# Kernel tuning notes

Hardware: AMD Instinct MI355X
Metric: run time of the kernel (lower is better)

The kernel has to match this reference:

```python
import jax, jax.numpy as jnp
import numpy as np

T, D_IN, H, KV, HD = 1024, 2048, 32, 8, 64
GROUP = H // KV  # 4
EPS = 1e-6


def _rmsnorm(x, w):
    inv_rms = jax.lax.rsqrt(jnp.mean(x * x, axis=-1, keepdims=True) + EPS)
    return x * inv_rms * w


def _rope(x, cos, sin):
    # x: [heads, T, HD]; cos/sin: [T, HD]
    hd = x.shape[-1]
    x1, x2 = x[..., : hd // 2], x[..., hd // 2 :]
    rotated = jnp.concatenate([-x2, x1], axis=-1)
    return x * cos[None, :, :] + rotated * sin[None, :, :]


def setup_inputs() -> dict:
    key = jax.random.key(0)
    ks = jax.random.split(key, 6)
    x = jax.random.normal(ks[0], (T, D_IN), dtype=jnp.float32)
    # RoPE tables (cos/sin over [T, HD])
    inv_freq = 1.0 / (10000.0 ** (np.arange(0, HD, 2, dtype=np.float64) / HD))
    ang = np.arange(T, dtype=np.float64)[:, None] * inv_freq[None, :]
    emb = np.concatenate([ang, ang], axis=-1)
    cos = jnp.asarray(np.cos(emb), dtype=jnp.float32)
    sin = jnp.asarray(np.sin(emb), dtype=jnp.float32)
    # causal mask: True above diagonal -> masked to -inf
    mask = jnp.triu(jnp.ones((T, T), dtype=jnp.bool_), k=1)
    # kaiming_normal fan_in (relu): std = sqrt(2/fan_in)
    Wq = jax.random.normal(ks[1], (H * HD, D_IN), jnp.float32) * (2.0 / D_IN) ** 0.5
    Wk = jax.random.normal(ks[2], (KV * HD, D_IN), jnp.float32) * (2.0 / D_IN) ** 0.5
    Wv = jax.random.normal(ks[3], (KV * HD, D_IN), jnp.float32) * (2.0 / D_IN) ** 0.5
    Wo = jax.random.normal(ks[4], (D_IN, H * HD), jnp.float32) * (2.0 / (H * HD)) ** 0.5
    q_norm_w = jnp.ones((HD,), jnp.float32)
    k_norm_w = jnp.ones((HD,), jnp.float32)
    one = jnp.ones((1,), jnp.float32)
    return {
        "x": x, "scale_x": one, "mask": mask,
        "cos": cos, "scale_cos": one, "sin": sin, "scale_sin": one,
        "Wq": Wq, "Wk": Wk, "Wv": Wv, "Wo": Wo,
        "q_norm_w": q_norm_w, "k_norm_w": k_norm_w,
    }


def reference(x, scale_x, mask, cos, scale_cos, sin, scale_sin,
              Wq, Wk, Wv, Wo, q_norm_w, k_norm_w):
    num_tokens = x.shape[0]
    # QKV projections
    q = (x @ Wq.T).reshape(num_tokens, H, HD).transpose(1, 0, 2)   # [H, T, HD]
    k = (x @ Wk.T).reshape(num_tokens, KV, HD).transpose(1, 0, 2)  # [KV, T, HD]
    v = (x @ Wv.T).reshape(num_tokens, KV, HD).transpose(1, 0, 2)  # [KV, T, HD]
    # qk_norm
    q = _rmsnorm(q, q_norm_w)
    k = _rmsnorm(k, k_norm_w)
    # RoPE
    q = _rope(q, cos, sin)
    k = _rope(k, cos, sin)
    # expand KV groups to all heads (repeat_interleave along head axis)
    k = jnp.repeat(k, GROUP, axis=0)  # [H, T, HD]
    v = jnp.repeat(v, GROUP, axis=0)  # [H, T, HD]
    # attention scores
    qk = jnp.einsum("htd,hsd->hts", q, k) / (HD ** 0.5)
    qk = jnp.where(mask[None, :, :], -jnp.inf, qk)
    attn = jax.nn.softmax(qk, axis=-1)
    out = jnp.einsum("hts,hsd->htd", attn, v)          # [H, T, HD]
    out = out.transpose(1, 0, 2).reshape(num_tokens, H * HD)
    return out @ Wo.T  # [T, D_IN]
```

## Files before the change

kernel.cpp:

```cpp
#include <hip/hip_runtime.h>

typedef __bf16 bf16x8 __attribute__((ext_vector_type(8)));
typedef float f32x4 __attribute__((ext_vector_type(4)));

#define T_TOK 1024
#define DIN   2048
#define NH    32
#define NKV   8
#define HD    64

__device__ __forceinline__ unsigned short f2bf(float f) {
  unsigned int u = __float_as_uint(f);
  unsigned int r = (u + 0x7fffu + ((u >> 16) & 1u)) >> 16;
  return (unsigned short)r;
}

__device__ __forceinline__ void glds16(const void* g, void* lds) {
  __builtin_amdgcn_global_load_lds(
      (const __attribute__((address_space(1))) void*)g,
      (__attribute__((address_space(3))) void*)lds, 16, 0, 0);
}

__global__ __launch_bounds__(256) void k_cvt_all(
    const float* __restrict__ x,  const float* __restrict__ wq,
    const float* __restrict__ wk, const float* __restrict__ wv,
    const float* __restrict__ wo, unsigned short* __restrict__ xb,
    unsigned short* __restrict__ wqkv, unsigned short* __restrict__ wob) {
  const long NX = 1l << 21, NWQ = 1l << 22, NWK = 1l << 20, NWV = 1l << 20;
  long i4 = ((long)blockIdx.x * blockDim.x + threadIdx.x) * 4;
  const float* src;
  unsigned short* dst;
  long off;
  if (i4 < NX)                       { src = x;  dst = xb;   off = i4; }
  else if (i4 < NX + NWQ)            { src = wq; dst = wqkv; off = i4 - NX; }
  else if (i4 < NX + NWQ + NWK)      { src = wk; dst = wqkv + NWQ; off = i4 - NX - NWQ; }
  else if (i4 < NX + NWQ + NWK + NWV){ src = wv; dst = wqkv + NWQ + NWK; off = i4 - NX - NWQ - NWK; }
  else                               { src = wo; dst = wob;  off = i4 - NX - NWQ - NWK - NWV; }
  float4 v = *reinterpret_cast<const float4*>(src + off);
  ushort4 o;
  o.x = f2bf(v.x); o.y = f2bf(v.y); o.z = f2bf(v.z); o.w = f2bf(v.w);
  *reinterpret_cast<ushort4*>(dst + off) = o;
}

template<int BM, int BN>
__global__ __launch_bounds__(256) void k_gemm3(
    const unsigned short* __restrict__ A, const unsigned short* __restrict__ B,
    float* __restrict__ C, int N, int K) {
  constexpr int NI = BM / 32;
  constexpr int NJ = BN / 32;
  __shared__ unsigned short As[4][BM * 64];
  __shared__ unsigned short Bs[4][BN * 64];
  const int lane = threadIdx.x & 63;
  const int wave = threadIdx.x >> 6;
  const int wm = wave >> 1, wn = wave & 1;
  const int lr = lane & 15, lk = lane >> 4;
  const int brow = blockIdx.y * BM;
  const int bcol = blockIdx.x * BN;

  const int srow = lane >> 3;
  const int scol = ((lane & 7) ^ srow) * 8;
  const unsigned short* Ag = A + (long)(brow + srow) * K + scol;
  const unsigned short* Bg = B + (long)(bcol + srow) * K + scol;

  f32x4 acc[NI][NJ];
#pragma unroll
  for (int i = 0; i < NI; i++)
#pragma unroll
    for (int j = 0; j < NJ; j++) acc[i][j] = (f32x4){0.f, 0.f, 0.f, 0.f};

  const int swz = (lr & 7) << 4;
  const int nt = K / 64;

#define GSTAGE(buf, tt) do {                                                   \
    const int kk_ = (tt) * 64;                                                 \
    _Pragma("unroll") for (int i_ = 0; i_ < NI; i_++) {                        \
      int strip = i_ * 4 + wave;                                               \
      glds16(Ag + (long)strip * 8 * K + kk_, (char*)As[buf] + strip * 1024);   \
    }                                                                          \
    _Pragma("unroll") for (int i_ = 0; i_ < NJ; i_++) {                        \
      int strip = i_ * 4 + wave;                                               \
      glds16(Bg + (long)strip * 8 * K + kk_, (char*)Bs[buf] + strip * 1024);   \
    }                                                                          \
  } while (0)

  GSTAGE(0, 0);
  GSTAGE(1, 1);
  GSTAGE(2, 2);

  for (int t = 0; t < nt; t++) {
    if (t + 2 < nt)      { asm volatile("s_waitcnt vmcnt(16)" ::: "memory"); }
    else if (t + 1 < nt) { asm volatile("s_waitcnt vmcnt(8)"  ::: "memory"); }
    else                 { asm volatile("s_waitcnt vmcnt(0)"  ::: "memory"); }
    __builtin_amdgcn_sched_barrier(0);
    __builtin_amdgcn_s_barrier();
    if (t + 3 < nt) GSTAGE((t + 3) & 3, t + 3);
    const int cur = t & 3;
#pragma unroll
    for (int s = 0; s < 2; s++) {
      bf16x8 a[NI], b[NJ];
#pragma unroll
      for (int i = 0; i < NI; i++) {
        int row = wm * (BM / 2) + i * 16 + lr;
        a[i] = *reinterpret_cast<const bf16x8*>(
            (const char*)As[cur] + row * 128 + ((s * 64 + lk * 16) ^ swz));
      }
#pragma unroll
      for (int j = 0; j < NJ; j++) {
        int row = wn * (BN / 2) + j * 16 + lr;
        b[j] = *reinterpret_cast<const bf16x8*>(
            (const char*)Bs[cur] + row * 128 + ((s * 64 + lk * 16) ^ swz));
      }
      __builtin_amdgcn_s_setprio(1);
#pragma unroll
      for (int i = 0; i < NI; i++)
#pragma unroll
        for (int j = 0; j < NJ; j++)
          acc[i][j] = __builtin_amdgcn_mfma_f32_16x16x32_bf16(a[i], b[j], acc[i][j], 0, 0, 0);
      __builtin_amdgcn_s_setprio(0);
    }
  }
#undef GSTAGE

#pragma unroll
  for (int i = 0; i < NI; i++)
#pragma unroll
    for (int j = 0; j < NJ; j++)
#pragma unroll
      for (int p = 0; p < 4; p++)
        C[(long)(brow + wm * (BM / 2) + i * 16 + lk * 4 + p) * N +
          (bcol + wn * (BN / 2) + j * 16 + lr)] = acc[i][j][p];
}

__global__ void k_norm_rope(const float* __restrict__ qkv_lin,
                            unsigned short* __restrict__ qb, unsigned short* __restrict__ kb,
                            const float* __restrict__ cosT, const float* __restrict__ sinT,
                            const float* __restrict__ qw, const float* __restrict__ kw) {
  int gw = (blockIdx.x * blockDim.x + threadIdx.x) >> 6;
  int lane = threadIdx.x & 63;
  int t = gw / (NH + NKV);
  int hh = gw % (NH + NKV);
  if (t >= T_TOK) return;
  const float* base;
  unsigned short* ob;
  const float* w;
  if (hh < NH) {
    base = qkv_lin + (long)t * 3072 + hh * HD;
    ob   = qb + (long)t * (NH * HD) + hh * HD;
    w = qw;
  } else {
    int kh = hh - NH;
    base = qkv_lin + (long)t * 3072 + 2048 + kh * HD;
    ob   = kb + (long)t * (NKV * HD) + kh * HD;
    w = kw;
  }
  float v = base[lane];
  float ss = v * v;
#pragma unroll
  for (int off = 1; off < 64; off <<= 1) ss += __shfl_xor(ss, off);
  float xn = v * rsqrtf(ss * (1.0f / HD) + 1e-6f) * w[lane];
  float other = __shfl_xor(xn, 32);
  float c = cosT[t * HD + lane], s = sinT[t * HD + lane];
  ob[lane] = f2bf(xn * c + (lane < 32 ? -other : other) * s);
}

__global__ __launch_bounds__(256) void k_vt(const float* __restrict__ qkv_lin,
                                            unsigned short* __restrict__ out) {
  __shared__ float t[32][33];
  int tx = threadIdx.x & 31, ty = threadIdx.x >> 5;
  int r0 = blockIdx.y * 32;
  int c0 = blockIdx.x * 32;
#pragma unroll
  for (int r = 0; r < 4; r++)
    t[ty + r * 8][tx] = qkv_lin[(long)(r0 + ty + r * 8) * 3072 + 2560 + c0 + tx];
  __syncthreads();
#pragma unroll
  for (int r = 0; r < 4; r++)
    out[(long)(c0 + ty + r * 8) * 1024 + r0 + tx] = f2bf(t[tx][ty + r * 8]);
}

__global__ __launch_bounds__(256) void k_flash(
    const unsigned short* __restrict__ qb, const unsigned short* __restrict__ kb,
    const unsigned short* __restrict__ vtb, unsigned short* __restrict__ ao) {
  __shared__ unsigned short Ks[4][64 * 64];
  __shared__ unsigned short Vs[4][64 * 64];
  __shared__ unsigned short plds[4][16 * 64];
  const int rb = 63 - blockIdx.x;
  const int kvh = blockIdx.y;
  const int lane = threadIdx.x & 63;
  const int wave = threadIdx.x >> 6;
  const int h = kvh * 4 + wave;
  const int lr = lane & 15, lk = lane >> 4;
  const int qrow = rb * 16;
  const int qt = rb >> 2;
  const int qrel = (rb & 3) * 16 + lr;
  const int pswz = (lr & 7) << 4;
  char* pbase = (char*)plds[wave];
  const float SC = 0.125f * 1.44269504f;
  const f32x4 z4 = {0.f, 0.f, 0.f, 0.f};

  const int srow = lane >> 3;
  const int scol = ((lane & 7) ^ srow) * 8;

#define STAGE(buf, tt) do {                                                    \
    _Pragma("unroll") for (int s_ = 0; s_ < 2; s_++) {                         \
      int strip = s_ * 4 + wave;                                               \
      glds16(kb + (long)((tt) * 64 + strip * 8 + srow) * 512 + kvh * 64 + scol,\
             (char*)Ks[buf] + strip * 1024);                                   \
      glds16(vtb + (long)(kvh * 64 + strip * 8 + srow) * 1024 + (tt) * 64 + scol,\
             (char*)Vs[buf] + strip * 1024);                                   \
    }                                                                          \
  } while (0)

  const unsigned short* qp = qb + (long)(qrow + lr) * (NH * HD) + h * HD + lk * 8;
  bf16x8 qa0 = *reinterpret_cast<const bf16x8*>(qp);
  bf16x8 qa1 = *reinterpret_cast<const bf16x8*>(qp + 32);

  f32x4 o[4];
#pragma unroll
  for (int f = 0; f < 4; f++) o[f] = z4;
  float m2 = -3.0e38f;
  float lp = 0.f;

  const int ntiles = qt + 1;
  STAGE(0, 0);
  if (ntiles > 1) STAGE(1, 1);
  if (ntiles > 2) STAGE(2, 2);

  for (int t = 0; t < ntiles; t++) {
    if (t + 2 < ntiles)      { asm volatile("s_waitcnt vmcnt(8)" ::: "memory"); }
    else if (t + 1 < ntiles) { asm volatile("s_waitcnt vmcnt(4)" ::: "memory"); }
    else                     { asm volatile("s_waitcnt vmcnt(0)" ::: "memory"); }
    __builtin_amdgcn_sched_barrier(0);
    __builtin_amdgcn_s_barrier();
    if (t + 3 < ntiles) STAGE((t + 3) & 3, t + 3);
    const int cur = t & 3;
    bf16x8 kf0[4], kf1[4];
#pragma unroll
    for (int f = 0; f < 4; f++) {
      const char* kbase = (const char*)Ks[cur] + (f * 16 + lr) * 128;
      kf0[f] = *reinterpret_cast<const bf16x8*>(kbase + ((lk * 16) ^ pswz));
      kf1[f] = *reinterpret_cast<const bf16x8*>(kbase + ((64 + lk * 16) ^ pswz));
    }
    f32x4 sacc[4];
    __builtin_amdgcn_s_setprio(1);
#pragma unroll
    for (int f = 0; f < 4; f++) {
      sacc[f] = __builtin_amdgcn_mfma_f32_16x16x32_bf16(kf0[f], qa0, z4, 0, 0, 0);
      sacc[f] = __builtin_amdgcn_mfma_f32_16x16x32_bf16(kf1[f], qa1, sacc[f], 0, 0, 0);
    }
    __builtin_amdgcn_s_setprio(0);
    const bool diag = (t == qt);
    float tmax = -3.0e38f;
#pragma unroll
    for (int f = 0; f < 4; f++)
#pragma unroll
      for (int p = 0; p < 4; p++) {
        float s_ = sacc[f][p] * SC;
        if (diag && (f * 16 + lk * 4 + p) > qrel) s_ = -3.0e38f;
        sacc[f][p] = s_;
        tmax = fmaxf(tmax, s_);
      }
    tmax = fmaxf(tmax, __shfl_xor(tmax, 16));
    tmax = fmaxf(tmax, __shfl_xor(tmax, 32));
    float mn = fmaxf(m2, tmax);
    float r = exp2f(m2 - mn);
    m2 = mn;
    float rp[4];
#pragma unroll
    for (int p = 0; p < 4; p++)
      rp[p] = __shfl(r, (lane & 48) | (lk * 4 + p));
    float ps = 0.f;
#pragma unroll
    for (int f = 0; f < 4; f++) {
      float e0 = exp2f(sacc[f][0] - mn), e1 = exp2f(sacc[f][1] - mn);
      float e2 = exp2f(sacc[f][2] - mn), e3 = exp2f(sacc[f][3] - mn);
      ps += (e0 + e1) + (e2 + e3);
      uint2 pk;
      pk.x = (unsigned)f2bf(e0) | ((unsigned)f2bf(e1) << 16);
      pk.y = (unsigned)f2bf(e2) | ((unsigned)f2bf(e3) << 16);
      *reinterpret_cast<uint2*>(pbase + lr * 128 + ((f * 32 + lk * 8) ^ pswz)) = pk;
    }
    lp = lp * r + ps;
#pragma unroll
    for (int fd = 0; fd < 4; fd++)
#pragma unroll
      for (int p = 0; p < 4; p++) o[fd][p] *= rp[p];
    bf16x8 vfr[8];
#pragma unroll
    for (int fd = 0; fd < 4; fd++) {
      const char* vbase = (const char*)Vs[cur] + (fd * 16 + lr) * 128;
      vfr[fd]     = *reinterpret_cast<const bf16x8*>(vbase + ((lk * 16) ^ pswz));
      vfr[4 + fd] = *reinterpret_cast<const bf16x8*>(vbase + ((64 + lk * 16) ^ pswz));
    }
    __builtin_amdgcn_s_setprio(1);
#pragma unroll
    for (int ks = 0; ks < 2; ks++) {
      bf16x8 pa = *reinterpret_cast<const bf16x8*>(
          pbase + lr * 128 + ((ks * 64 + lk * 16) ^ pswz));
#pragma unroll
      for (int fd = 0; fd < 4; fd++)
        o[fd] = __builtin_amdgcn_mfma_f32_16x16x32_bf16(pa, vfr[ks * 4 + fd], o[fd], 0, 0, 0);
    }
    __builtin_amdgcn_s_setprio(0);
  }
#undef STAGE

  lp += __shfl_xor(lp, 16);
  lp += __shfl_xor(lp, 32);
  float lo[4];
#pragma unroll
  for (int p = 0; p < 4; p++) lo[p] = __shfl(lp, (lane & 48) | (lk * 4 + p));
#pragma unroll
  for (int fd = 0; fd < 4; fd++)
#pragma unroll
    for (int p = 0; p < 4; p++) {
      int qg = qrow + lk * 4 + p;
      int d = fd * 16 + lr;
      ao[(long)qg * (NH * HD) + h * HD + d] = f2bf(o[fd][p] / lo[p]);
    }
}

extern "C" void kernel_launch(void* const* d_in, const int* in_sizes, int n_in,
                              void* d_out, int out_size, void* d_ws, size_t ws_size,
                              hipStream_t stream) {
  const float* x    = (const float*)d_in[0];
  const float* cosT = (const float*)d_in[3];
  const float* sinT = (const float*)d_in[5];
  const float* Wq   = (const float*)d_in[7];
  const float* Wk   = (const float*)d_in[8];
  const float* Wv   = (const float*)d_in[9];
  const float* Wo   = (const float*)d_in[10];
  const float* qw   = (const float*)d_in[11];
  const float* kw   = (const float*)d_in[12];
  float* out = (float*)d_out;

  char* ws = (char*)d_ws;
  unsigned short* xb    = (unsigned short*)(ws);
  unsigned short* Wqkv  = (unsigned short*)(ws + (4u << 20));
  unsigned short* Wob   = (unsigned short*)(ws + (16u << 20));
  float* qkv_lin = (float*)(ws + (24u << 20));
  unsigned short* qbb = (unsigned short*)(ws + (36u << 20));
  unsigned short* kbb = (unsigned short*)(ws + (40u << 20));
  unsigned short* vtb = (unsigned short*)(ws + (41u << 20));
  unsigned short* ao  = (unsigned short*)(ws + (42u << 20));

  k_cvt_all<<<12288, 256, 0, stream>>>(x, Wq, Wk, Wv, Wo, xb, Wqkv, Wob);

  k_gemm3<128, 128><<<dim3(24, 8), 256, 0, stream>>>(xb, Wqkv, qkv_lin, 3072, 2048);

  k_norm_rope<<<(T_TOK * (NH + NKV) * 64) / 256, 256, 0, stream>>>(
      qkv_lin, qbb, kbb, cosT, sinT, qw, kw);

  k_vt<<<dim3(16, 32), 256, 0, stream>>>(qkv_lin, vtb);

  k_flash<<<dim3(64, 8), 256, 0, stream>>>(qbb, kbb, vtb, ao);

  k_gemm3<128, 128><<<dim3(16, 8), 256, 0, stream>>>(ao, Wob, out, 2048, 2048);
}
```

Measured before the change: 218.9 us.

## Fuse QK RMSNorm, RoPE and V transpose into QKV GEMM epilogue

Moves the Q/K RMSNorm and RoPE plus the V transpose into the QKV GEMM epilogue, dropping the fp32 qkv_lin intermediate and two kernel launches. GEMM tiles shrink to 64x128 with a 3-stage instead of 4-stage LDS pipeline, doubling grid size for better CU occupancy on both GEMMs. The epilogue now does cross-lane shuffles and scattered bf16 stores. Lower LDS use allows more resident blocks, but the shallower prefetch exposes more memory latency.

```diff
diff --git a/kernel.cpp b/kernel.cpp
--- a/kernel.cpp
+++ b/kernel.cpp
@@ -42,14 +42,19 @@
   *reinterpret_cast<ushort4*>(dst + off) = o;
 }
 
-template<int BM, int BN>
+template<int BM, int BN, int MODE>
 __global__ __launch_bounds__(256) void k_gemm3(
     const unsigned short* __restrict__ A, const unsigned short* __restrict__ B,
-    float* __restrict__ C, int N, int K) {
+    float* __restrict__ C, int N, int K,
+    unsigned short* __restrict__ qb, unsigned short* __restrict__ kbo,
+    unsigned short* __restrict__ vtb, const float* __restrict__ cosT,
+    const float* __restrict__ sinT, const float* __restrict__ qw,
+    const float* __restrict__ kw) {
   constexpr int NI = BM / 32;
   constexpr int NJ = BN / 32;
-  __shared__ unsigned short As[4][BM * 64];
-  __shared__ unsigned short Bs[4][BN * 64];
+  static_assert(NI + NJ == 6, "vmcnt literals assume 6 loads/batch/wave");
+  __shared__ unsigned short As[3][BM * 64];
+  __shared__ unsigned short Bs[3][BN * 64];
   const int lane = threadIdx.x & 63;
   const int wave = threadIdx.x >> 6;
   const int wm = wave >> 1, wn = wave & 1;
@@ -85,16 +90,14 @@
 
   GSTAGE(0, 0);
   GSTAGE(1, 1);
-  GSTAGE(2, 2);
 
   for (int t = 0; t < nt; t++) {
-    if (t + 2 < nt)      { asm volatile("s_waitcnt vmcnt(16)" ::: "memory"); }
-    else if (t + 1 < nt) { asm volatile("s_waitcnt vmcnt(8)"  ::: "memory"); }
-    else                 { asm volatile("s_waitcnt vmcnt(0)"  ::: "memory"); }
+    if (t + 1 < nt) { asm volatile("s_waitcnt vmcnt(6)" ::: "memory"); }
+    else            { asm volatile("s_waitcnt vmcnt(0)" ::: "memory"); }
     __builtin_amdgcn_sched_barrier(0);
     __builtin_amdgcn_s_barrier();
-    if (t + 3 < nt) GSTAGE((t + 3) & 3, t + 3);
-    const int cur = t & 3;
+    if (t + 2 < nt) GSTAGE((t + 2) % 3, t + 2);
+    const int cur = t % 3;
 #pragma unroll
     for (int s = 0; s < 2; s++) {
       bf16x8 a[NI], b[NJ];
@@ -121,61 +124,68 @@
   }
 #undef GSTAGE
 
-#pragma unroll
-  for (int i = 0; i < NI; i++)
-#pragma unroll
-    for (int j = 0; j < NJ; j++)
-#pragma unroll
-      for (int p = 0; p < 4; p++)
-        C[(long)(brow + wm * (BM / 2) + i * 16 + lk * 4 + p) * N +
-          (bcol + wn * (BN / 2) + j * 16 + lr)] = acc[i][j][p];
-}
-
-__global__ void k_norm_rope(const float* __restrict__ qkv_lin,
-                            unsigned short* __restrict__ qb, unsigned short* __restrict__ kb,
-                            const float* __restrict__ cosT, const float* __restrict__ sinT,
-                            const float* __restrict__ qw, const float* __restrict__ kw) {
-  int gw = (blockIdx.x * blockDim.x + threadIdx.x) >> 6;
-  int lane = threadIdx.x & 63;
-  int t = gw / (NH + NKV);
-  int hh = gw % (NH + NKV);
-  if (t >= T_TOK) return;
-  const float* base;
-  unsigned short* ob;
-  const float* w;
-  if (hh < NH) {
-    base = qkv_lin + (long)t * 3072 + hh * HD;
-    ob   = qb + (long)t * (NH * HD) + hh * HD;
-    w = qw;
+  if constexpr (MODE == 1) {
+    const int colbase = bcol + wn * 64;
+    if (colbase < 2560) {
+      const bool isQ = (colbase < 2048);
+      const float* w = isQ ? qw : kw;
+      unsigned short* dst = isQ ? qb : kbo;
+      const int dN = isQ ? (NH * HD) : (NKV * HD);
+      const int dcol = isQ ? colbase : colbase - 2048;
+      float wv[NJ];
+#pragma unroll
+      for (int j = 0; j < NJ; j++) wv[j] = w[j * 16 + lr];
+#pragma unroll
+      for (int i = 0; i < NI; i++) {
+#pragma unroll
+        for (int p = 0; p < 4; p++) {
+          float s2 = 0.f;
+#pragma unroll
+          for (int j = 0; j < NJ; j++) s2 += acc[i][j][p] * acc[i][j][p];
+          s2 += __shfl_xor(s2, 1);
+          s2 += __shfl_xor(s2, 2);
+          s2 += __shfl_xor(s2, 4);
+          s2 += __shfl_xor(s2, 8);
+          const float inv = rsqrtf(s2 * (1.0f / HD) + 1e-6f);
+          const int t = brow + wm * (BM / 2) + i * 16 + lk * 4 + p;
+#pragma unroll
+          for (int j = 0; j < NJ; j++) {
+            const int hd = j * 16 + lr;
+            const float xn = acc[i][j][p] * inv * wv[j];
+            const int jp = (j < 2) ? j + 2 : j - 2;
+            float rot = acc[i][jp][p] * inv * wv[jp];
+            if (j < 2) rot = -rot;
+            const float c = cosT[t * HD + hd], s = sinT[t * HD + hd];
+            dst[(long)t * dN + dcol + hd] = f2bf(xn * c + rot * s);
+          }
+        }
+      }
+    } else {
+#pragma unroll
+      for (int i = 0; i < NI; i++) {
+        const int t0 = brow + wm * (BM / 2) + i * 16 + lk * 4;
+#pragma unroll
+        for (int j = 0; j < NJ; j++) {
+          const int c = colbase - 2560 + j * 16 + lr;
+          ushort4 pk;
+          pk.x = f2bf(acc[i][j][0]);
+          pk.y = f2bf(acc[i][j][1]);
+          pk.z = f2bf(acc[i][j][2]);
+          pk.w = f2bf(acc[i][j][3]);
+          *reinterpret_cast<ushort4*>(vtb + (long)c * T_TOK + t0) = pk;
+        }
+      }
+    }
   } else {
-    int kh = hh - NH;
-    base = qkv_lin + (long)t * 3072 + 2048 + kh * HD;
-    ob   = kb + (long)t * (NKV * HD) + kh * HD;
-    w = kw;
+#pragma unroll
+    for (int i = 0; i < NI; i++)
+#pragma unroll
+      for (int j = 0; j < NJ; j++)
+#pragma unroll
+        for (int p = 0; p < 4; p++)
+          C[(long)(brow + wm * (BM / 2) + i * 16 + lk * 4 + p) * N +
+            (bcol + wn * (BN / 2) + j * 16 + lr)] = acc[i][j][p];
   }
-  float v = base[lane];
-  float ss = v * v;
-#pragma unroll
-  for (int off = 1; off < 64; off <<= 1) ss += __shfl_xor(ss, off);
-  float xn = v * rsqrtf(ss * (1.0f / HD) + 1e-6f) * w[lane];
-  float other = __shfl_xor(xn, 32);
-  float c = cosT[t * HD + lane], s = sinT[t * HD + lane];
-  ob[lane] = f2bf(xn * c + (lane < 32 ? -other : other) * s);
-}
-
-__global__ __launch_bounds__(256) void k_vt(const float* __restrict__ qkv_lin,
-                                            unsigned short* __restrict__ out) {
-  __shared__ float t[32][33];
-  int tx = threadIdx.x & 31, ty = threadIdx.x >> 5;
-  int r0 = blockIdx.y * 32;
-  int c0 = blockIdx.x * 32;
-#pragma unroll
-  for (int r = 0; r < 4; r++)
-    t[ty + r * 8][tx] = qkv_lin[(long)(r0 + ty + r * 8) * 3072 + 2560 + c0 + tx];
-  __syncthreads();
-#pragma unroll
-  for (int r = 0; r < 4; r++)
-    out[(long)(c0 + ty + r * 8) * 1024 + r0 + tx] = f2bf(t[tx][ty + r * 8]);
 }
 
 __global__ __launch_bounds__(256) void k_flash(
@@ -338,22 +348,19 @@
   unsigned short* xb    = (unsigned short*)(ws);
   unsigned short* Wqkv  = (unsigned short*)(ws + (4u << 20));
   unsigned short* Wob   = (unsigned short*)(ws + (16u << 20));
-  float* qkv_lin = (float*)(ws + (24u << 20));
-  unsigned short* qbb = (unsigned short*)(ws + (36u << 20));
-  unsigned short* kbb = (unsigned short*)(ws + (40u << 20));
-  unsigned short* vtb = (unsigned short*)(ws + (41u << 20));
-  unsigned short* ao  = (unsigned short*)(ws + (42u << 20));
+  unsigned short* qbb = (unsigned short*)(ws + (24u << 20));
+  unsigned short* kbb = (unsigned short*)(ws + (28u << 20));
+  unsigned short* vtb = (unsigned short*)(ws + (29u << 20));
+  unsigned short* ao  = (unsigned short*)(ws + (30u << 20));
 
   k_cvt_all<<<12288, 256, 0, stream>>>(x, Wq, Wk, Wv, Wo, xb, Wqkv, Wob);
 
-  k_gemm3<128, 128><<<dim3(24, 8), 256, 0, stream>>>(xb, Wqkv, qkv_lin, 3072, 2048);
-
-  k_norm_rope<<<(T_TOK * (NH + NKV) * 64) / 256, 256, 0, stream>>>(
-      qkv_lin, qbb, kbb, cosT, sinT, qw, kw);
-
-  k_vt<<<dim3(16, 32), 256, 0, stream>>>(qkv_lin, vtb);
+  k_gemm3<64, 128, 1><<<dim3(24, 16), 256, 0, stream>>>(
+      xb, Wqkv, nullptr, 3072, 2048, qbb, kbb, vtb, cosT, sinT, qw, kw);
 
   k_flash<<<dim3(64, 8), 256, 0, stream>>>(qbb, kbb, vtb, ao);
 
-  k_gemm3<128, 128><<<dim3(16, 8), 256, 0, stream>>>(ao, Wob, out, 2048, 2048);
-}
+  k_gemm3<64, 128, 0><<<dim3(16, 16), 256, 0, stream>>>(
+      ao, Wob, out, 2048, 2048, nullptr, nullptr, nullptr, nullptr, nullptr,
+      nullptr, nullptr);
+}
```

New measurement: 199.3 us. 8.9% less time.
